# Kernel tuning notes

Hardware: AMD Instinct MI355X
Metric: run time of the kernel (lower is better)

## Reference

```python
import jax, jax.numpy as jnp
import numpy as np

R = 0.2          # stable-distribution hash bucket width
TABLE_SIZE = 2   # hash table size (buckets)
M = 5            # number of appended ALSH transform dims
EPS = 1e-12


def conv2d(x, W, b, pad):
    out = jax.lax.conv_general_dilated(
        x, W, window_strides=(1, 1), padding=[(pad, pad), (pad, pad)],
        dimension_numbers=('NCHW', 'OIHW', 'NCHW'))
    return out + b[None, :, None, None]


def maxpool2(x):
    return jax.lax.reduce_window(x, -jnp.inf, jax.lax.max,
                                 (1, 1, 2, 2), (1, 1, 2, 2), 'VALID')


def alsh_mask(x, W, a, c):
    """ALSH filter selection: hash P(kernels) and Q(query) with a stable
    distribution hash h(v)=floor((a.v+b)/r) mod table_size; active filters
    are those landing in the query's bucket. Returns [B, Cout] 0/1 mask.
    Multiplying conv output by this mask == gather active filters then
    zero_fill_missing back to full channel count."""
    Cout, Cin, kH, kW = W.shape
    Kf = W.reshape(Cout, -1)                       # [Cout, Cin*kH*kW]
    norms = jnp.linalg.norm(Kf, axis=1)
    Kn = Kf / (jnp.max(norms) + EPS)               # scale so all norms <= 1
    n = jnp.linalg.norm(Kn, axis=1, keepdims=True)
    # P transform: append norm^2, norm^4, ..., norm^(2^M)
    powers = jnp.concatenate([n ** (2 ** (i + 1)) for i in range(M)], axis=1)
    P = jnp.concatenate([Kn, powers], axis=1)      # [Cout, d+M]
    kh = jnp.mod(jnp.floor((P @ a + c[0]) / R), TABLE_SIZE)  # [Cout]
    # query vector: per-sample channel means broadcast over kernel support
    cm = x.mean(axis=(2, 3))                       # [B, Cin]
    q = jnp.repeat(cm, kH * kW, axis=1)            # [B, Cin*kH*kW] (cin,kh,kw order)
    qn = q / (jnp.linalg.norm(q, axis=1, keepdims=True) + EPS)
    # Q transform: append M halves
    Qv = jnp.concatenate([qn, jnp.full((q.shape[0], M), 0.5, q.dtype)], axis=1)
    qh = jnp.mod(jnp.floor((Qv @ a + c[0]) / R), TABLE_SIZE)  # [B]
    return (kh[None, :] == qh[:, None]).astype(x.dtype)       # [B, Cout]


def setup_inputs() -> dict:
    key = jax.random.key(0)
    ks = jax.random.split(key, 16)
    u = lambda k, s: jax.random.uniform(k, s, jnp.float32, 0.0, R)
    n = lambda k, s, sc=0.1: jax.random.normal(k, s, jnp.float32) * sc
    return {
        'x': jax.random.normal(ks[0], (4096, 3, 32, 32), jnp.float32),
        'W1': n(ks[1], (16, 3, 5, 5)), 'b1': n(ks[2], (16,)),
        'a1': jax.random.normal(ks[3], (80,), jnp.float32), 'c1': u(ks[4], (1,)),
        'W2': n(ks[5], (20, 16, 5, 5)), 'b2': n(ks[6], (20,)),
        'a2': jax.random.normal(ks[7], (405,), jnp.float32), 'c2': u(ks[8], (1,)),
        'W3': n(ks[9], (20, 20, 5, 5)), 'b3': n(ks[10], (20,)),
        'a3': jax.random.normal(ks[11], (505,), jnp.float32), 'c3': u(ks[12], (1,)),
        'Wo': n(ks[13], (10, 320)), 'bo': n(ks[14], (10,)),
    }


def reference(x, W1, b1, a1, c1, W2, b2, a2, c2, W3, b3, a3, c3, Wo, bo):
    m1 = alsh_mask(x, W1, a1, c1)
    h = jax.nn.relu(conv2d(x, W1, b1, 2)) * m1[:, :, None, None]
    h = maxpool2(h)                                # [B,16,16,16]
    m2 = alsh_mask(h, W2, a2, c2)
    h = jax.nn.relu(conv2d(h, W2, b2, 2)) * m2[:, :, None, None]
    h = maxpool2(h)                                # [B,20,8,8]
    m3 = alsh_mask(h, W3, a3, c3)
    h = jax.nn.relu(conv2d(h, W3, b3, 2)) * m3[:, :, None, None]
    # zero_fill_missing -> identity here: inactive channels already zero
    h = maxpool2(h)                                # [B,20,4,4]
    flat = h.reshape(h.shape[0], -1)               # [B,320]
    return flat @ Wo.T + bo
```

## Files before the change

kernel.cpp:

```cpp
#include <hip/hip_runtime.h>
#include <hip/hip_bf16.h>

#define EPSV 1e-12
#define RHASH 0.2

__device__ __forceinline__ int fmod2(double t) {
    return (int)(((long long)floor(t)) & 1LL);
}

__device__ __forceinline__ void load_row6(const float* base, float* r) {
    float2 a0 = *(const float2*)(base);
    float2 a1 = *(const float2*)(base + 2);
    float2 a2 = *(const float2*)(base + 4);
    r[0] = a0.x; r[1] = a0.y; r[2] = a1.x; r[3] = a1.y; r[4] = a2.x; r[5] = a2.y;
}

__device__ __forceinline__ void load_row12(const float* base, float* r) {
    #pragma unroll
    for (int j = 0; j < 6; ++j) *(float2*)&r[2 * j] = *(const float2*)(base + 2 * j);
}

#define FMA4(c,kx,w) { float wg=(w); \
  acc[c][0]=fmaf(wg,cur[kx],acc[c][0]); acc[c][1]=fmaf(wg,cur[(kx)+1],acc[c][1]); \
  acc[c][2]=fmaf(wg,nxt[kx],acc[c][2]); acc[c][3]=fmaf(wg,nxt[(kx)+1],acc[c][3]); }

__device__ void layer_setup(const float* W, const float* a, double cval,
                            int Co, int Ci, int* kh, double* asum, double* qc,
                            double* s_norm, float* Wbuf, float* abuf)
{
    const int t = threadIdx.x;
    const int D = Ci * 25;
    for (int i = t; i < Co * D; i += 256) Wbuf[i] = W[i];
    for (int i = t; i < D + 5; i += 256) abuf[i] = a[i];
    __syncthreads();
    if (t < Co) {
        double s = 0;
        for (int j = 0; j < D; ++j) { double w = (double)Wbuf[t * D + j]; s += w * w; }
        s_norm[t] = sqrt(s);
    }
    __syncthreads();
    if (t == 0) {
        double mx = 0;
        for (int i = 0; i < Co; ++i) mx = fmax(mx, s_norm[i]);
        s_norm[23] = 1.0 / (mx + EPSV);
    }
    __syncthreads();
    double scale = s_norm[23];
    if (t < Co) {
        double dp = 0;
        for (int j = 0; j < D; ++j) dp += (double)Wbuf[t * D + j] * (double)abuf[j];
        dp *= scale;
        double n = s_norm[t] * scale;
        double p = n * n;
        for (int m = 0; m < 5; ++m) { dp += p * (double)abuf[D + m]; p *= p; }
        kh[t] = fmod2((dp + cval) / RHASH);
    }
    if (t >= 64 && t < 64 + Ci) {
        int c = t - 64;
        double s = 0;
        for (int j = 0; j < 25; ++j) s += (double)abuf[c * 25 + j];
        asum[c] = s;
    }
    if (t == 128) {
        double s = 0;
        for (int m = 0; m < 5; ++m) s += (double)abuf[D + m];
        *qc = 0.5 * s + cval;
    }
    __syncthreads();
}

__global__ __launch_bounds__(256) void prep_kernel(
    const float* W1, const float* a1, const float* c1,
    const float* W2, const float* a2, const float* c2,
    const float* W3, const float* a3, const float* c3,
    double* dmeta, int* imeta,
    float* Wp1, float* Wp2, float* Wp3)
{
    __shared__ float Wbuf[10000];
    __shared__ float abuf[512];
    __shared__ double s_norm[24];
    const int blk = blockIdx.x;
    if (blk == 0) {
        layer_setup(W1, a1, (double)c1[0], 16, 3,  imeta + 0,  dmeta + 0,  dmeta + 39, s_norm, Wbuf, abuf);
    } else if (blk == 1) {
        layer_setup(W2, a2, (double)c2[0], 20, 16, imeta + 16, dmeta + 3,  dmeta + 40, s_norm, Wbuf, abuf);
    } else if (blk == 2) {
        layer_setup(W3, a3, (double)c3[0], 20, 20, imeta + 36, dmeta + 19, dmeta + 41, s_norm, Wbuf, abuf);
    } else {
        int i = (blk - 3) * 256 + threadIdx.x;
        if (i < 1200) {
            int co = i & 15, r = i >> 4;
            int kx = r % 5, r2 = r / 5, ky = r2 % 5, ci = r2 / 5;
            Wp1[i] = W1[co * 75 + ci * 25 + ky * 5 + kx];
        } else if (i < 1200 + 8960) {
            int k = i - 1200;
            int j = k % 28, r = k / 28;
            int cog = r % 4, r2 = r / 4, ky = r2 % 5, ci = r2 / 5;
            Wp2[k] = (j < 25) ? W2[(cog * 5 + j / 5) * 400 + ci * 25 + ky * 5 + (j % 5)] : 0.f;
        } else if (i < 1200 + 8960 + 11200) {
            int k = i - 10160;
            int j = k % 28, r = k / 28;
            int cog = r % 4, r2 = r / 4, ky = r2 % 5, ci = r2 / 5;
            Wp3[k] = (j < 25) ? W3[(cog * 5 + j / 5) * 500 + ci * 25 + ky * 5 + (j % 5)] : 0.f;
        }
    }
}

__global__ __launch_bounds__(256) void conv1_kernel(
    const float* __restrict__ x, const float* __restrict__ Wp1,
    const float* __restrict__ b1, const int* __restrict__ kh1,
    const double* __restrict__ dmeta, float* __restrict__ h1,
    int* __restrict__ qh2)
{
    __shared__ float xs[3][36][38];
    __shared__ float Ws[1200];
    __shared__ double s_red[3];
    __shared__ double s_ch[16][4];

    const int b = blockIdx.x, t = threadIdx.x;
    const int w = t >> 6, ln = t & 63;

    for (int i = t; i < 3 * 36 * 38; i += 256) (&xs[0][0][0])[i] = 0.f;
    for (int i = t; i < 600; i += 256) ((float2*)Ws)[i] = ((const float2*)Wp1)[i];
    __syncthreads();
    const float2* xb2 = (const float2*)(x + (size_t)b * 3072);
    for (int i = t; i < 1536; i += 256) {
        int c = i >> 9, rem = i & 511;
        int row = rem >> 4, col2 = rem & 15;
        *(float2*)&xs[c][row + 2][col2 * 2 + 2] = xb2[i];
    }
    __syncthreads();

    if (w < 3) {
        double s = 0;
        for (int j = 0; j < 16; ++j) {
            int i = ln + 64 * j;
            s += (double)xs[w][(i >> 5) + 2][(i & 31) + 2];
        }
        #pragma unroll
        for (int off = 32; off; off >>= 1) s += __shfl_xor(s, off);
        if (ln == 0) s_red[w] = s;
    }
    __syncthreads();
    double dp = 0, nn = 0;
    #pragma unroll
    for (int c = 0; c < 3; ++c) {
        double cm = s_red[c] * (1.0 / 1024.0);
        dp += cm * dmeta[c]; nn += cm * cm;
    }
    const int qh = fmod2((dp / (5.0 * sqrt(nn) + EPSV) + dmeta[39]) / RHASH);

    const int cog = ln >> 4;
    const int py = 4 * w + ((ln >> 2) & 3), pxg = ln & 3;
    const int y0 = 2 * py, x0 = 8 * pxg;

    float accA[4][8], accB[4][8];
    #pragma unroll
    for (int c = 0; c < 4; ++c) {
        float bb = b1[cog * 4 + c];
        #pragma unroll
        for (int k = 0; k < 8; ++k) { accA[c][k] = bb; accB[c][k] = bb; }
    }

    #pragma unroll
    for (int ci = 0; ci < 3; ++ci) {
        float ra[12], rb[12];
        load_row12(&xs[ci][y0][x0],     ra);
        load_row12(&xs[ci][y0 + 1][x0], rb);
        #pragma unroll
        for (int ky = 0; ky < 5; ++ky) {
            const float4* wq = (const float4*)&Ws[((ci * 5 + ky) * 5) * 16 + cog * 4];
            #pragma unroll
            for (int kx = 0; kx < 5; ++kx) {
                float4 wv = wq[kx * 4];
                { float wg = wv.x;
                  #pragma unroll
                  for (int k = 0; k < 8; ++k) { accA[0][k] = fmaf(wg, ra[k + kx], accA[0][k]);
                                                accB[0][k] = fmaf(wg, rb[k + kx], accB[0][k]); } }
                { float wg = wv.y;
                  #pragma unroll
                  for (int k = 0; k < 8; ++k) { accA[1][k] = fmaf(wg, ra[k + kx], accA[1][k]);
                                                accB[1][k] = fmaf(wg, rb[k + kx], accB[1][k]); } }
                { float wg = wv.z;
                  #pragma unroll
                  for (int k = 0; k < 8; ++k) { accA[2][k] = fmaf(wg, ra[k + kx], accA[2][k]);
                                                accB[2][k] = fmaf(wg, rb[k + kx], accB[2][k]); } }
                { float wg = wv.w;
                  #pragma unroll
                  for (int k = 0; k < 8; ++k) { accA[3][k] = fmaf(wg, ra[k + kx], accA[3][k]);
                                                accB[3][k] = fmaf(wg, rb[k + kx], accB[3][k]); } }
            }
            if (ky < 4) {
                #pragma unroll
                for (int j = 0; j < 12; ++j) ra[j] = rb[j];
                load_row12(&xs[ci][y0 + ky + 2][x0], rb);
            }
        }
    }

    float* hb = h1 + (size_t)b * 4096 + py * 16 + pxg * 4;
    double csum[4];
    #pragma unroll
    for (int c = 0; c < 4; ++c) {
        int co = cog * 4 + c;
        float mask = (kh1[co] == qh) ? 1.f : 0.f;
        float v0 = fmaxf(fmaxf(accA[c][0], accA[c][1]), fmaxf(accB[c][0], accB[c][1]));
        float v1 = fmaxf(fmaxf(accA[c][2], accA[c][3]), fmaxf(accB[c][2], accB[c][3]));
        float v2 = fmaxf(fmaxf(accA[c][4], accA[c][5]), fmaxf(accB[c][4], accB[c][5]));
        float v3 = fmaxf(fmaxf(accA[c][6], accA[c][7]), fmaxf(accB[c][6], accB[c][7]));
        v0 = fmaxf(v0, 0.f) * mask; v1 = fmaxf(v1, 0.f) * mask;
        v2 = fmaxf(v2, 0.f) * mask; v3 = fmaxf(v3, 0.f) * mask;
        *(float4*)(hb + co * 256) = make_float4(v0, v1, v2, v3);
        csum[c] = (double)v0 + (double)v1 + (double)v2 + (double)v3;
    }
    #pragma unroll
    for (int c = 0; c < 4; ++c) {
        double s = csum[c];
        s += __shfl_xor(s, 8); s += __shfl_xor(s, 4);
        s += __shfl_xor(s, 2); s += __shfl_xor(s, 1);
        if ((ln & 15) == 0) s_ch[cog * 4 + c][w] = s;
    }
    __syncthreads();
    if (t == 0) {
        double dp2 = 0, nn2 = 0;
        #pragma unroll
        for (int c = 0; c < 16; ++c) {
            double cm = (s_ch[c][0] + s_ch[c][1] + s_ch[c][2] + s_ch[c][3]) * (1.0 / 256.0);
            dp2 += cm * dmeta[3 + c]; nn2 += cm * cm;
        }
        qh2[b] = fmod2((dp2 / (5.0 * sqrt(nn2) + EPSV) + dmeta[40]) / RHASH);
    }
}

#define XSP(si,ci,row,col) (u + (((si) * 4 + (ci)) * 20 + (row)) * 22 + (col))

#define C2_XLOAD(CH, RX) { \
    _Pragma("unroll") \
    for (int j = 0; j < 8; ++j) { \
        int i = t + 256 * j, si = i >> 9, rem = i & 511, cil = rem >> 7, rr = rem & 127; \
        RX[j] = (b0 + si < B) ? ((const float2*)h1)[(size_t)(b0 + si) * 2048 + ((CH) * 4 + cil) * 128 + rr] \
                              : make_float2(0.f, 0.f); \
    } }

#define C2_XCOMMIT(RX) { \
    _Pragma("unroll") \
    for (int j = 0; j < 8; ++j) { \
        int i = t + 256 * j, si = i >> 9, rem = i & 511, cil = rem >> 7, rr = rem & 127; \
        int p2 = rr * 2, row = p2 >> 4, col = p2 & 15; \
        *(float2*)XSP(si, cil, row + 2, col + 2) = RX[j]; \
    } }

__global__ __launch_bounds__(256) void conv23_kernel(
    const float* __restrict__ h1, const float* __restrict__ Wp2,
    const float* __restrict__ b2, const float* __restrict__ b3,
    const int* __restrict__ imeta, const int* __restrict__ qh2,
    const double* __restrict__ dmeta, const float* __restrict__ Wp3,
    const float* __restrict__ Wo, const float* __restrict__ bo,
    float* __restrict__ out, int B)
{
    __shared__ float u[9280];
    __shared__ double s_ch[4][20];
    __shared__ int s_qh[4];

    const int b0 = blockIdx.x * 4, t = threadIdx.x;
    const int s = t >> 6, l = t & 63;
    const int cog = l >> 4, pos = l & 15;
    const int b = b0 + s;
    const bool valid = (b < B);

    const int py2 = pos >> 1, pxg = pos & 1;
    float* Ws2 = u + 7040;
    const int* kh2 = imeta + 16;

    for (int i = t; i < 7040; i += 256) u[i] = 0.f;

    const int qh = valid ? qh2[b] : 0;
    float accA[5][8], accB[5][8];
    #pragma unroll
    for (int c = 0; c < 5; ++c) {
        float bb = b2[cog * 5 + c];
        #pragma unroll
        for (int k = 0; k < 8; ++k) { accA[c][k] = bb; accB[c][k] = bb; }
    }

    float2 rx[8];
    C2_XLOAD(0, rx);
    __syncthreads();

    for (int ch = 0; ch < 4; ++ch) {
        for (int i = t; i < 1120; i += 256)
            ((float2*)Ws2)[i] = ((const float2*)(Wp2 + ch * 2240))[i];
        C2_XCOMMIT(rx);
        __syncthreads();
        if (ch < 3) C2_XLOAD(ch + 1, rx);

        for (int cil = 0; cil < 4; ++cil) {
            float ra[12], rb[12];
            load_row12(XSP(s, cil, 2 * py2, 8 * pxg),     ra);
            load_row12(XSP(s, cil, 2 * py2 + 1, 8 * pxg), rb);
            #pragma unroll
            for (int ky = 0; ky < 5; ++ky) {
                float wv[28];
                const float4* wp = (const float4*)&Ws2[((cil * 5 + ky) * 4 + cog) * 28];
                *(float4*)&wv[0]  = wp[0];
                *(float4*)&wv[4]  = wp[1];
                *(float4*)&wv[8]  = wp[2];
                *(float4*)&wv[12] = wp[3];
                *(float4*)&wv[16] = wp[4];
                *(float4*)&wv[20] = wp[5];
                *(float4*)&wv[24] = wp[6];
                #pragma unroll
                for (int c = 0; c < 5; ++c) {
                    #pragma unroll
                    for (int kx = 0; kx < 5; ++kx) {
                        float wg = wv[c * 5 + kx];
                        #pragma unroll
                        for (int k = 0; k < 8; ++k) {
                            accA[c][k] = fmaf(wg, ra[k + kx], accA[c][k]);
                            accB[c][k] = fmaf(wg, rb[k + kx], accB[c][k]);
                        }
                    }
                }
                if (ky < 4) {
                    #pragma unroll
                    for (int j = 0; j < 12; ++j) ra[j] = rb[j];
                    load_row12(XSP(s, cil, 2 * py2 + ky + 2, 8 * pxg), rb);
                }
            }
        }
        __syncthreads();
    }

    float* h2s  = u;
    float* zrow = u + 8800;

    for (int i = t; i < 2560; i += 256) {
        int r = i >> 2, hc = i & 3;
        u[r * 12 + ((hc < 2) ? hc : hc + 8)] = 0.f;
    }
    if (t < 12) zrow[t] = 0.f;

    double csum[5];
    #pragma unroll
    for (int c = 0; c < 5; ++c) {
        int co = cog * 5 + c;
        float mask = (kh2[co] == qh) ? 1.f : 0.f;
        float v0 = fmaxf(fmaxf(accA[c][0], accA[c][1]), fmaxf(accB[c][0], accB[c][1]));
        float v1 = fmaxf(fmaxf(accA[c][2], accA[c][3]), fmaxf(accB[c][2], accB[c][3]));
        float v2 = fmaxf(fmaxf(accA[c][4], accA[c][5]), fmaxf(accB[c][4], accB[c][5]));
        float v3 = fmaxf(fmaxf(accA[c][6], accA[c][7]), fmaxf(accB[c][6], accB[c][7]));
        v0 = fmaxf(v0, 0.f) * mask; v1 = fmaxf(v1, 0.f) * mask;
        v2 = fmaxf(v2, 0.f) * mask; v3 = fmaxf(v3, 0.f) * mask;
        int base = ((s * 20 + co) * 8 + py2) * 12 + 2 + pxg * 4;
        *(float2*)&u[base]     = make_float2(v0, v1);
        *(float2*)&u[base + 2] = make_float2(v2, v3);
        csum[c] = (double)v0 + (double)v1 + (double)v2 + (double)v3;
    }
    #pragma unroll
    for (int c = 0; c < 5; ++c) {
        double sv = csum[c];
        sv += __shfl_xor(sv, 8); sv += __shfl_xor(sv, 4);
        sv += __shfl_xor(sv, 2); sv += __shfl_xor(sv, 1);
        if (pos == 0) s_ch[s][cog * 5 + c] = sv;
    }
    __syncthreads();
    if (l == 0) {
        double dp2 = 0, nn2 = 0;
        #pragma unroll
        for (int c = 0; c < 20; ++c) {
            double cm = s_ch[s][c] * (1.0 / 64.0);
            dp2 += cm * dmeta[19 + c]; nn2 += cm * cm;
        }
        s_qh[s] = fmod2((dp2 / (5.0 * sqrt(nn2) + EPSV) + dmeta[41]) / RHASH);
    }

    const int* kh3 = imeta + 36;
    const int py3 = pos >> 2, px3 = pos & 3;
    const int r0 = 2 * py3 - 2;
    const int x0 = 2 * px3;
    float* Ws3 = u + 7680;

    float acc[5][4];
    #pragma unroll
    for (int c = 0; c < 5; ++c) {
        float bb = b3[cog * 5 + c];
        acc[c][0] = bb; acc[c][1] = bb; acc[c][2] = bb; acc[c][3] = bb;
    }

    for (int ch = 0; ch < 10; ++ch) {
        __syncthreads();
        for (int i = t; i < 560; i += 256)
            ((float2*)Ws3)[i] = ((const float2*)(Wp3 + ch * 1120))[i];
        __syncthreads();

        #pragma unroll
        for (int ci2 = 0; ci2 < 2; ++ci2) {
            const int ci = ch * 2 + ci2;
            const float* rb0 = u + ((s * 20 + ci) * 8) * 12 + x0;
            float cur[6], nxt[6];
            { const float* p = (r0 >= 0 && r0 < 8) ? (rb0 + r0 * 12) : zrow;
              load_row6(p, cur); }
            { int r = r0 + 1; const float* p = (r >= 0 && r < 8) ? (rb0 + r * 12) : zrow;
              load_row6(p, nxt); }
            #pragma unroll
            for (int ky = 0; ky < 5; ++ky) {
                const float* wrow = &Ws3[((ci2 * 5 + ky) * 4 + cog) * 28];
                const float4* wq = (const float4*)wrow;
                float4 q;
                q = wq[0]; FMA4(0, 0, q.x) FMA4(0, 1, q.y) FMA4(0, 2, q.z) FMA4(0, 3, q.w)
                q = wq[1]; FMA4(0, 4, q.x) FMA4(1, 0, q.y) FMA4(1, 1, q.z) FMA4(1, 2, q.w)
                q = wq[2]; FMA4(1, 3, q.x) FMA4(1, 4, q.y) FMA4(2, 0, q.z) FMA4(2, 1, q.w)
                q = wq[3]; FMA4(2, 2, q.x) FMA4(2, 3, q.y) FMA4(2, 4, q.z) FMA4(3, 0, q.w)
                q = wq[4]; FMA4(3, 1, q.x) FMA4(3, 2, q.y) FMA4(3, 3, q.z) FMA4(3, 4, q.w)
                q = wq[5]; FMA4(4, 0, q.x) FMA4(4, 1, q.y) FMA4(4, 2, q.z) FMA4(4, 3, q.w)
                FMA4(4, 4, wrow[24])
                if (ky < 4) {
                    #pragma unroll
                    for (int j = 0; j < 6; ++j) cur[j] = nxt[j];
                    int r = r0 + ky + 2;
                    const float* p = (r >= 0 && r < 8) ? (rb0 + r * 12) : zrow;
                    load_row6(p, nxt);
                }
            }
        }
    }

    const int qh3v = s_qh[s];
    float pv[5];
    #pragma unroll
    for (int c = 0; c < 5; ++c) {
        float m = fmaxf(fmaxf(acc[c][0], acc[c][1]), fmaxf(acc[c][2], acc[c][3]));
        pv[c] = fmaxf(m, 0.f) * ((kh3[cog * 5 + c] == qh3v) ? 1.f : 0.f);
    }
    #pragma unroll
    for (int o = 0; o < 10; ++o) {
        float p = 0.f;
        #pragma unroll
        for (int c = 0; c < 5; ++c)
            p = fmaf(pv[c], Wo[o * 320 + (cog * 5 + c) * 16 + pos], p);
        p += __shfl_xor(p, 32); p += __shfl_xor(p, 16); p += __shfl_xor(p, 8);
        p += __shfl_xor(p, 4);  p += __shfl_xor(p, 2);  p += __shfl_xor(p, 1);
        if (l == 0 && valid) out[(size_t)b * 10 + o] = p + bo[o];
    }
}

extern "C" void kernel_launch(void* const* d_in, const int* in_sizes, int n_in,
                              void* d_out, int out_size, void* d_ws, size_t ws_size,
                              hipStream_t stream)
{
    const float* x  = (const float*)d_in[0];
    const float* W1 = (const float*)d_in[1];
    const float* b1 = (const float*)d_in[2];
    const float* a1 = (const float*)d_in[3];
    const float* c1 = (const float*)d_in[4];
    const float* W2 = (const float*)d_in[5];
    const float* b2 = (const float*)d_in[6];
    const float* a2 = (const float*)d_in[7];
    const float* c2 = (const float*)d_in[8];
    const float* W3 = (const float*)d_in[9];
    const float* b3 = (const float*)d_in[10];
    const float* a3 = (const float*)d_in[11];
    const float* c3 = (const float*)d_in[12];
    const float* Wo = (const float*)d_in[13];
    const float* bo = (const float*)d_in[14];
    float* out = (float*)d_out;

    const int B = in_sizes[0] / 3072;

    float* h1  = (float*)d_ws;
    float* h2  = h1 + (size_t)B * 4096;
    float* Wp1 = h2 + (size_t)B * 1280;
    float* Wp2 = Wp1 + 1200;
    float* Wp3 = Wp2 + 8960;
    double* dmeta = (double*)(Wp3 + 11200);
    int* imeta = (int*)(dmeta + 42);
    int* qh2 = imeta + 56;

    prep_kernel<<<87, 256, 0, stream>>>(W1, a1, c1, W2, a2, c2, W3, a3, c3,
                                        dmeta, imeta, Wp1, Wp2, Wp3);
    conv1_kernel<<<B, 256, 0, stream>>>(x, Wp1, b1, imeta, dmeta, h1, qh2);
    conv23_kernel<<<(B + 3) / 4, 256, 0, stream>>>(h1, Wp2, b2, b3, imeta, qh2,
                                                   dmeta, Wp3, Wo, bo, out, B);
}
```

Measured before the change: 530.1 us.

## Drop register prefetch of conv2 input and stage conv3 weights in larger chunks

Removes the register double-buffered prefetch of conv2 input tiles and instead loads each chunk directly from global into shared memory before the barrier. This lowers register pressure from the eight float2 prefetch registers. It also doubles the conv3 weight chunk size (4 input channels per stage instead of 2), halving the number of barrier pairs at the cost of more shared memory (u grows, zrow moves to its own array). Losing the prefetch exposes global load latency at each conv2 chunk.

```diff
diff --git a/kernel.cpp b/kernel.cpp
--- a/kernel.cpp
+++ b/kernel.cpp
@@ -234,22 +234,6 @@
 
 #define XSP(si,ci,row,col) (u + (((si) * 4 + (ci)) * 20 + (row)) * 22 + (col))
 
-#define C2_XLOAD(CH, RX) { \
-    _Pragma("unroll") \
-    for (int j = 0; j < 8; ++j) { \
-        int i = t + 256 * j, si = i >> 9, rem = i & 511, cil = rem >> 7, rr = rem & 127; \
-        RX[j] = (b0 + si < B) ? ((const float2*)h1)[(size_t)(b0 + si) * 2048 + ((CH) * 4 + cil) * 128 + rr] \
-                              : make_float2(0.f, 0.f); \
-    } }
-
-#define C2_XCOMMIT(RX) { \
-    _Pragma("unroll") \
-    for (int j = 0; j < 8; ++j) { \
-        int i = t + 256 * j, si = i >> 9, rem = i & 511, cil = rem >> 7, rr = rem & 127; \
-        int p2 = rr * 2, row = p2 >> 4, col = p2 & 15; \
-        *(float2*)XSP(si, cil, row + 2, col + 2) = RX[j]; \
-    } }
-
 __global__ __launch_bounds__(256) void conv23_kernel(
     const float* __restrict__ h1, const float* __restrict__ Wp2,
     const float* __restrict__ b2, const float* __restrict__ b3,
@@ -258,9 +242,10 @@
     const float* __restrict__ Wo, const float* __restrict__ bo,
     float* __restrict__ out, int B)
 {
-    __shared__ float u[9280];
+    __shared__ float u[9920];
     __shared__ double s_ch[4][20];
     __shared__ int s_qh[4];
+    __shared__ float zrow[12];
 
     const int b0 = blockIdx.x * 4, t = threadIdx.x;
     const int s = t >> 6, l = t & 63;
@@ -282,17 +267,19 @@
         #pragma unroll
         for (int k = 0; k < 8; ++k) { accA[c][k] = bb; accB[c][k] = bb; }
     }
-
-    float2 rx[8];
-    C2_XLOAD(0, rx);
     __syncthreads();
 
     for (int ch = 0; ch < 4; ++ch) {
         for (int i = t; i < 1120; i += 256)
             ((float2*)Ws2)[i] = ((const float2*)(Wp2 + ch * 2240))[i];
-        C2_XCOMMIT(rx);
+        for (int i = t; i < 2048; i += 256) {
+            int si = i >> 9, rem = i & 511, cil = rem >> 7, rr = rem & 127;
+            int p2 = rr * 2, row = p2 >> 4, col = p2 & 15;
+            if (b0 + si < B)
+                *(float2*)XSP(si, cil, row + 2, col + 2) =
+                    ((const float2*)h1)[(size_t)(b0 + si) * 2048 + (ch * 4 + cil) * 128 + rr];
+        }
         __syncthreads();
-        if (ch < 3) C2_XLOAD(ch + 1, rx);
 
         for (int cil = 0; cil < 4; ++cil) {
             float ra[12], rb[12];
@@ -331,9 +318,6 @@
         __syncthreads();
     }
 
-    float* h2s  = u;
-    float* zrow = u + 8800;
-
     for (int i = t; i < 2560; i += 256) {
         int r = i >> 2, hc = i & 3;
         u[r * 12 + ((hc < 2) ? hc : hc + 8)] = 0.f;
@@ -387,15 +371,15 @@
         acc[c][0] = bb; acc[c][1] = bb; acc[c][2] = bb; acc[c][3] = bb;
     }
 
-    for (int ch = 0; ch < 10; ++ch) {
+    for (int ch = 0; ch < 5; ++ch) {
         __syncthreads();
-        for (int i = t; i < 560; i += 256)
-            ((float2*)Ws3)[i] = ((const float2*)(Wp3 + ch * 1120))[i];
+        for (int i = t; i < 1120; i += 256)
+            ((float2*)Ws3)[i] = ((const float2*)(Wp3 + ch * 2240))[i];
         __syncthreads();
 
         #pragma unroll
-        for (int ci2 = 0; ci2 < 2; ++ci2) {
-            const int ci = ch * 2 + ci2;
+        for (int ci4 = 0; ci4 < 4; ++ci4) {
+            const int ci = ch * 4 + ci4;
             const float* rb0 = u + ((s * 20 + ci) * 8) * 12 + x0;
             float cur[6], nxt[6];
             { const float* p = (r0 >= 0 && r0 < 8) ? (rb0 + r0 * 12) : zrow;
@@ -404,7 +388,7 @@
               load_row6(p, nxt); }
             #pragma unroll
             for (int ky = 0; ky < 5; ++ky) {
-                const float* wrow = &Ws3[((ci2 * 5 + ky) * 4 + cog) * 28];
+                const float* wrow = &Ws3[((ci4 * 5 + ky) * 4 + cog) * 28];
                 const float4* wq = (const float4*)wrow;
                 float4 q;
                 q = wq[0]; FMA4(0, 0, q.x) FMA4(0, 1, q.y) FMA4(0, 2, q.z) FMA4(0, 3, q.w)
```

After: 559.0 us. +5.4%, slower.
